# Kernel tuning notes

Hardware: AMD Instinct MI355X
Metric: run time of the kernel (lower is better)

The kernel has to match this reference:

```python
import jax, jax.numpy as jnp
import numpy as np

FEATURE_DIM, HIDDEN_DIM, ATTN_DIM = 2048, 1024, 1024
B, L = 128, 196


def setup_inputs() -> dict:
    key = jax.random.key(0)
    ks = jax.random.split(key, 8)
    s_enc = 1.0 / np.sqrt(FEATURE_DIM)
    s_hid = 1.0 / np.sqrt(HIDDEN_DIM)
    s_full = 1.0 / np.sqrt(ATTN_DIM)
    return {
        "encoder_out": jax.random.normal(ks[0], (B, L, FEATURE_DIM), jnp.float32),
        "hidden": jax.random.normal(ks[1], (B, HIDDEN_DIM), jnp.float32),
        "W_enc": jax.random.uniform(ks[2], (FEATURE_DIM, ATTN_DIM), jnp.float32, -s_enc, s_enc),
        "b_enc": jax.random.uniform(ks[3], (ATTN_DIM,), jnp.float32, -s_enc, s_enc),
        "W_hid": jax.random.uniform(ks[4], (HIDDEN_DIM, ATTN_DIM), jnp.float32, -s_hid, s_hid),
        "b_hid": jax.random.uniform(ks[5], (ATTN_DIM,), jnp.float32, -s_hid, s_hid),
        "W_full": jax.random.uniform(ks[6], (ATTN_DIM,), jnp.float32, -s_full, s_full),
        "b_full": jax.random.uniform(ks[7], (1,), jnp.float32, -s_full, s_full),
    }


def reference(encoder_out, hidden, W_enc, b_enc, W_hid, b_hid, W_full, b_full):
    # attn1: (B, L, A)
    attn1 = jnp.einsum("blf,fa->bla", encoder_out, W_enc) + b_enc
    # attn2: (B, 1, A)
    attn2 = (hidden @ W_hid + b_hid)[:, None, :]
    attn = jax.nn.relu(attn1 + attn2)
    # scalar score per location: (B, L)
    scores = jnp.einsum("bla,a->bl", attn, W_full) + b_full[0]
    alpha = jax.nn.softmax(scores, axis=1)
    # weighted sum over L: (B, F)
    context = jnp.einsum("blf,bl->bf", encoder_out, alpha)
    return context, alpha
```

## Files before the change

kernel.cpp:

```cpp
#include <hip/hip_runtime.h>
#include <hip/hip_bf16.h>

typedef unsigned short u16;
typedef short s16x8 __attribute__((ext_vector_type(8)));
typedef float f32x4 __attribute__((ext_vector_type(4)));

#define F_DIM 2048
#define A_DIM 1024
#define H_DIM 1024
#define BATCH 128
#define LLEN  196
#define MROWS (BATCH * LLEN)
#define LDA   40

__device__ __forceinline__ u16 f2b(float x) {
  union { float f; unsigned int u; } c; c.f = x;
  unsigned int r = (c.u + 0x7fffu + ((c.u >> 16) & 1u)) >> 16;
  return (u16)r;
}

__global__ void wenc_cvt_kernel(const float* __restrict__ W, u16* __restrict__ WT) {
  __shared__ float tile[32][33];
  int kb = blockIdx.x * 32, ab = blockIdx.y * 32;
  int t = threadIdx.x;
  int r = t >> 3, c = (t & 7) * 4;
  float4 v = *(const float4*)&W[(size_t)(kb + r) * A_DIM + ab + c];
  tile[r][c] = v.x; tile[r][c + 1] = v.y; tile[r][c + 2] = v.z; tile[r][c + 3] = v.w;
  __syncthreads();
  ushort4 o;
  o.x = f2b(tile[c + 0][r]);
  o.y = f2b(tile[c + 1][r]);
  o.z = f2b(tile[c + 2][r]);
  o.w = f2b(tile[c + 3][r]);
  *(ushort4*)&WT[(size_t)(ab + r) * F_DIM + kb + c] = o;
}

__global__ void attn2_kernel(const float* __restrict__ hidden, const float* __restrict__ W_hid,
                             const float* __restrict__ b_hid, const float* __restrict__ b_enc,
                             float* __restrict__ attn2p) {
  __shared__ float hl[8][256];
  int t = threadIdx.x;
  int a  = blockIdx.x * 256 + t;
  int b0 = blockIdx.y * 8;
  int k0 = blockIdx.z * 256;
  {
    int j = t >> 5, kk = (t & 31) * 8;
    float4 v0 = *(const float4*)&hidden[(size_t)(b0 + j) * H_DIM + k0 + kk];
    float4 v1 = *(const float4*)&hidden[(size_t)(b0 + j) * H_DIM + k0 + kk + 4];
    hl[j][kk + 0] = v0.x; hl[j][kk + 1] = v0.y; hl[j][kk + 2] = v0.z; hl[j][kk + 3] = v0.w;
    hl[j][kk + 4] = v1.x; hl[j][kk + 5] = v1.y; hl[j][kk + 6] = v1.z; hl[j][kk + 7] = v1.w;
  }
  __syncthreads();
  float acc[8] = {0.f, 0.f, 0.f, 0.f, 0.f, 0.f, 0.f, 0.f};
  #pragma unroll 4
  for (int k = 0; k < 256; ++k) {
    float w = W_hid[(size_t)(k0 + k) * A_DIM + a];
    #pragma unroll
    for (int j = 0; j < 8; ++j) acc[j] = fmaf(hl[j][k], w, acc[j]);
  }
  if (blockIdx.z == 0) {
    float bias = b_hid[a] + b_enc[a];
    #pragma unroll
    for (int j = 0; j < 8; ++j) acc[j] += bias;
  }
  #pragma unroll
  for (int j = 0; j < 8; ++j) atomicAdd(&attn2p[(size_t)(b0 + j) * A_DIM + a], acc[j]);
}

__global__ void gemm_score_kernel(const float* __restrict__ enc, const u16* __restrict__ WT,
                                  const float* __restrict__ attn2p, const float* __restrict__ W_full,
                                  float* __restrict__ scores) {
  __shared__ __align__(16) u16 As[128 * LDA];
  __shared__ __align__(16) u16 Bs[128 * LDA];
  __shared__ float wf_lds[128];
  __shared__ float at2_lds[2][128];

  int n0 = blockIdx.x * 128;
  int m0 = blockIdx.y * 128;
  int t = threadIdx.x;

  int b0 = m0 / LLEN;
  int bnd = (b0 + 1) * LLEN;
  int b1 = min(b0 + 1, BATCH - 1);

  if (t < 128) {
    wf_lds[t] = W_full[n0 + t];
    at2_lds[0][t] = attn2p[(size_t)b0 * A_DIM + n0 + t];
    at2_lds[1][t] = attn2p[(size_t)b1 * A_DIM + n0 + t];
  }

  int lane = t & 63, wave = t >> 6;
  int wr = wave >> 1, wc = wave & 1;
  int c16 = lane & 15, quad = lane >> 4;

  f32x4 acc[4][4];
  #pragma unroll
  for (int i = 0; i < 4; ++i)
    #pragma unroll
    for (int j = 0; j < 4; ++j) acc[i][j] = (f32x4){0.f, 0.f, 0.f, 0.f};

  int ar = t >> 3, ac = (t & 7) * 4;
  int br = t >> 2, bc = (t & 3) * 8;
  const float* ap = enc + (size_t)(m0 + ar) * F_DIM + ac;
  const u16*  bp = WT + (size_t)(n0 + br) * F_DIM + bc;

  for (int kt = 0; kt < F_DIM; kt += 32) {
    #pragma unroll
    for (int p = 0; p < 4; ++p) {
      float4 v = *(const float4*)(ap + (size_t)p * 32 * F_DIM + kt);
      ushort4 u;
      u.x = f2b(v.x); u.y = f2b(v.y); u.z = f2b(v.z); u.w = f2b(v.w);
      *(ushort4*)&As[(ar + p * 32) * LDA + ac] = u;
    }
    #pragma unroll
    for (int p = 0; p < 2; ++p) {
      uint4 v = *(const uint4*)(bp + (size_t)p * 64 * F_DIM + kt);
      *(uint4*)&Bs[(br + p * 64) * LDA + bc] = v;
    }
    __syncthreads();
    s16x8 af[4], bf[4];
    #pragma unroll
    for (int i = 0; i < 4; ++i) {
      af[i] = *(const s16x8*)&As[(wr * 64 + i * 16 + c16) * LDA + quad * 8];
      bf[i] = *(const s16x8*)&Bs[(wc * 64 + i * 16 + c16) * LDA + quad * 8];
    }
    #pragma unroll
    for (int mi = 0; mi < 4; ++mi)
      #pragma unroll
      for (int ni = 0; ni < 4; ++ni)
        acc[mi][ni] = __builtin_amdgcn_mfma_f32_16x16x32_bf16(af[mi], bf[ni], acc[mi][ni], 0, 0, 0);
    __syncthreads();
  }

  float wf[4], a2a[4], a2b[4];
  #pragma unroll
  for (int ni = 0; ni < 4; ++ni) {
    int col = wc * 64 + ni * 16 + c16;
    wf[ni] = wf_lds[col];
    a2a[ni] = at2_lds[0][col];
    a2b[ni] = at2_lds[1][col];
  }
  #pragma unroll
  for (int mi = 0; mi < 4; ++mi) {
    #pragma unroll
    for (int r = 0; r < 4; ++r) {
      int row_g = m0 + wr * 64 + mi * 16 + quad * 4 + r;
      bool hi = row_g >= bnd;
      float p = 0.f;
      #pragma unroll
      for (int ni = 0; ni < 4; ++ni) {
        float v = acc[mi][ni][r] + (hi ? a2b[ni] : a2a[ni]);
        v = fmaxf(v, 0.f);
        p = fmaf(v, wf[ni], p);
      }
      p += __shfl_xor(p, 1);
      p += __shfl_xor(p, 2);
      p += __shfl_xor(p, 4);
      p += __shfl_xor(p, 8);
      if (c16 == 0) atomicAdd(&scores[row_g], p);
    }
  }
}

__global__ void softmax_kernel(const float* __restrict__ scores, float* __restrict__ alpha) {
  __shared__ float red[8];
  int b = blockIdx.x, t = threadIdx.x;
  float s = (t < LLEN) ? scores[b * LLEN + t] : -3.0e38f;
  float m = s;
  #pragma unroll
  for (int o = 1; o <= 32; o <<= 1) m = fmaxf(m, __shfl_xor(m, o));
  if ((t & 63) == 0) red[t >> 6] = m;
  __syncthreads();
  m = fmaxf(fmaxf(red[0], red[1]), fmaxf(red[2], red[3]));
  float e = (t < LLEN) ? expf(s - m) : 0.f;
  float sum = e;
  #pragma unroll
  for (int o = 1; o <= 32; o <<= 1) sum += __shfl_xor(sum, o);
  __syncthreads();
  if ((t & 63) == 0) red[4 + (t >> 6)] = sum;
  __syncthreads();
  sum = red[4] + red[5] + red[6] + red[7];
  if (t < LLEN) alpha[b * LLEN + t] = e / sum;
}

__global__ void context_kernel(const float* __restrict__ enc, const float* __restrict__ alpha,
                               float* __restrict__ out) {
  __shared__ float al[LLEN];
  int b = blockIdx.y, t = threadIdx.x;
  int f4 = blockIdx.x * 256 + t;
  if (t < LLEN) al[t] = alpha[b * LLEN + t];
  __syncthreads();
  const float4* e4 = (const float4*)enc + (size_t)b * LLEN * (F_DIM / 4) + f4;
  float4 acc = {0.f, 0.f, 0.f, 0.f};
  #pragma unroll 4
  for (int l = 0; l < LLEN; ++l) {
    float4 v = e4[(size_t)l * (F_DIM / 4)];
    float a = al[l];
    acc.x = fmaf(v.x, a, acc.x);
    acc.y = fmaf(v.y, a, acc.y);
    acc.z = fmaf(v.z, a, acc.z);
    acc.w = fmaf(v.w, a, acc.w);
  }
  ((float4*)out)[(size_t)b * (F_DIM / 4) + f4] = acc;
}

extern "C" void kernel_launch(void* const* d_in, const int* in_sizes, int n_in,
                              void* d_out, int out_size, void* d_ws, size_t ws_size,
                              hipStream_t stream) {
  const float* enc    = (const float*)d_in[0];
  const float* hidden = (const float*)d_in[1];
  const float* W_enc  = (const float*)d_in[2];
  const float* b_enc  = (const float*)d_in[3];
  const float* W_hid  = (const float*)d_in[4];
  const float* b_hid  = (const float*)d_in[5];
  const float* W_full = (const float*)d_in[6];
  float* out = (float*)d_out;

  char* ws = (char*)d_ws;
  u16*   WT     = (u16*)ws;
  float* attn2p = (float*)(ws + (size_t)A_DIM * F_DIM * sizeof(u16));
  float* scores = (float*)(ws + (size_t)A_DIM * F_DIM * sizeof(u16) + (size_t)BATCH * A_DIM * sizeof(float));

  hipMemsetAsync(attn2p, 0, (size_t)BATCH * A_DIM * sizeof(float), stream);
  hipMemsetAsync(scores, 0, (size_t)MROWS * sizeof(float), stream);

  float* alpha_out = out + (size_t)BATCH * F_DIM;

  wenc_cvt_kernel<<<dim3(F_DIM / 32, A_DIM / 32), 256, 0, stream>>>(W_enc, WT);
  attn2_kernel<<<dim3(A_DIM / 256, BATCH / 8, 4), 256, 0, stream>>>(hidden, W_hid, b_hid, b_enc, attn2p);
  gemm_score_kernel<<<dim3(A_DIM / 128, MROWS / 128), 256, 0, stream>>>(enc, WT, attn2p, W_full, scores);
  softmax_kernel<<<dim3(BATCH), 256, 0, stream>>>(scores, alpha_out);
  context_kernel<<<dim3(F_DIM / 4 / 256, BATCH), 256, 0, stream>>>(enc, alpha_out, out);
}
```

Measured before the change: 575.3 us.

## Pre-convert encoder to bf16 and load GEMM tiles directly into LDS

Adds a pass that converts encoder_out to bf16 once into workspace, so the score GEMM no longer re-reads fp32 activations and converts them for every N-tile. The GEMM then uses global_load_lds to copy tiles straight into unpadded LDS. The context kernel is also split four ways over L and combined with atomics to expose more parallelism. This needs about 100MB of extra workspace, with a fallback to the old path if it is missing, and the unpadded LDS layout may cause bank conflicts.

```diff
diff --git a/kernel.cpp b/kernel.cpp
--- a/kernel.cpp
+++ b/kernel.cpp
@@ -19,6 +19,11 @@
   return (u16)r;
 }
 
+__device__ __forceinline__ void gload_lds16(const void* g, void* l) {
+  __builtin_amdgcn_global_load_lds((const __attribute__((address_space(1))) void*)g,
+                                   (__attribute__((address_space(3))) void*)l, 16, 0, 0);
+}
+
 __global__ void wenc_cvt_kernel(const float* __restrict__ W, u16* __restrict__ WT) {
   __shared__ float tile[32][33];
   int kb = blockIdx.x * 32, ab = blockIdx.y * 32;
@@ -33,6 +38,21 @@
   o.z = f2b(tile[c + 2][r]);
   o.w = f2b(tile[c + 3][r]);
   *(ushort4*)&WT[(size_t)(ab + r) * F_DIM + kb + c] = o;
+}
+
+__global__ void enc_cvt_kernel(const float* __restrict__ enc, u16* __restrict__ encb) {
+  int idx = blockIdx.x * 256 + threadIdx.x;
+  const float4* src = (const float4*)enc;
+  uint4* dst = (uint4*)encb;
+  #pragma unroll
+  for (int it = 0; it < 8; ++it) {
+    size_t p = (size_t)idx + (size_t)it * 802816;
+    float4 v0 = src[p * 2], v1 = src[p * 2 + 1];
+    union { u16 u[8]; uint4 q; } o;
+    o.u[0] = f2b(v0.x); o.u[1] = f2b(v0.y); o.u[2] = f2b(v0.z); o.u[3] = f2b(v0.w);
+    o.u[4] = f2b(v1.x); o.u[5] = f2b(v1.y); o.u[6] = f2b(v1.z); o.u[7] = f2b(v1.w);
+    dst[p] = o.q;
+  }
 }
 
 __global__ void attn2_kernel(const float* __restrict__ hidden, const float* __restrict__ W_hid,
@@ -67,11 +87,11 @@
   for (int j = 0; j < 8; ++j) atomicAdd(&attn2p[(size_t)(b0 + j) * A_DIM + a], acc[j]);
 }
 
-__global__ void gemm_score_kernel(const float* __restrict__ enc, const u16* __restrict__ WT,
-                                  const float* __restrict__ attn2p, const float* __restrict__ W_full,
-                                  float* __restrict__ scores) {
-  __shared__ __align__(16) u16 As[128 * LDA];
-  __shared__ __align__(16) u16 Bs[128 * LDA];
+__global__ void gemm_score_bf16(const u16* __restrict__ encb, const u16* __restrict__ WT,
+                                const float* __restrict__ attn2p, const float* __restrict__ W_full,
+                                float* __restrict__ scores) {
+  __shared__ __align__(16) u16 As[128 * 32];
+  __shared__ __align__(16) u16 Bs[128 * 32];
   __shared__ float wf_lds[128];
   __shared__ float at2_lds[2][128];
 
@@ -99,30 +119,24 @@
     #pragma unroll
     for (int j = 0; j < 4; ++j) acc[i][j] = (f32x4){0.f, 0.f, 0.f, 0.f};
 
-  int ar = t >> 3, ac = (t & 7) * 4;
-  int br = t >> 2, bc = (t & 3) * 8;
-  const float* ap = enc + (size_t)(m0 + ar) * F_DIM + ac;
-  const u16*  bp = WT + (size_t)(n0 + br) * F_DIM + bc;
+  const u16* agp0 = encb + (size_t)(m0 + (t >> 2)) * F_DIM + (t & 3) * 8;
+  const u16* agp1 = agp0 + (size_t)64 * F_DIM;
+  const u16* bgp0 = WT + (size_t)(n0 + (t >> 2)) * F_DIM + (t & 3) * 8;
+  const u16* bgp1 = bgp0 + (size_t)64 * F_DIM;
+  u16* al = As + wave * 512;
+  u16* bl = Bs + wave * 512;
 
   for (int kt = 0; kt < F_DIM; kt += 32) {
-    #pragma unroll
-    for (int p = 0; p < 4; ++p) {
-      float4 v = *(const float4*)(ap + (size_t)p * 32 * F_DIM + kt);
-      ushort4 u;
-      u.x = f2b(v.x); u.y = f2b(v.y); u.z = f2b(v.z); u.w = f2b(v.w);
-      *(ushort4*)&As[(ar + p * 32) * LDA + ac] = u;
-    }
-    #pragma unroll
-    for (int p = 0; p < 2; ++p) {
-      uint4 v = *(const uint4*)(bp + (size_t)p * 64 * F_DIM + kt);
-      *(uint4*)&Bs[(br + p * 64) * LDA + bc] = v;
-    }
+    gload_lds16(agp0 + kt, al);
+    gload_lds16(agp1 + kt, al + 2048);
+    gload_lds16(bgp0 + kt, bl);
+    gload_lds16(bgp1 + kt, bl + 2048);
     __syncthreads();
     s16x8 af[4], bf[4];
     #pragma unroll
     for (int i = 0; i < 4; ++i) {
-      af[i] = *(const s16x8*)&As[(wr * 64 + i * 16 + c16) * LDA + quad * 8];
-      bf[i] = *(const s16x8*)&Bs[(wc * 64 + i * 16 + c16) * LDA + quad * 8];
+      af[i] = *(const s16x8*)&As[(wr * 64 + i * 16 + c16) * 32 + quad * 8];
+      bf[i] = *(const s16x8*)&Bs[(wc * 64 + i * 16 + c16) * 32 + quad * 8];
     }
     #pragma unroll
     for (int mi = 0; mi < 4; ++mi)
@@ -162,6 +176,94 @@
   }
 }
 
+__global__ void gemm_score_f32(const float* __restrict__ enc, const u16* __restrict__ WT,
+                               const float* __restrict__ attn2p, const float* __restrict__ W_full,
+                               float* __restrict__ scores) {
+  __shared__ __align__(16) u16 As[128 * LDA];
+  __shared__ __align__(16) u16 Bs[128 * LDA];
+  __shared__ float wf_lds[128];
+  __shared__ float at2_lds[2][128];
+
+  int n0 = blockIdx.x * 128;
+  int m0 = blockIdx.y * 128;
+  int t = threadIdx.x;
+  int b0 = m0 / LLEN;
+  int bnd = (b0 + 1) * LLEN;
+  int b1 = min(b0 + 1, BATCH - 1);
+  if (t < 128) {
+    wf_lds[t] = W_full[n0 + t];
+    at2_lds[0][t] = attn2p[(size_t)b0 * A_DIM + n0 + t];
+    at2_lds[1][t] = attn2p[(size_t)b1 * A_DIM + n0 + t];
+  }
+  int lane = t & 63, wave = t >> 6;
+  int wr = wave >> 1, wc = wave & 1;
+  int c16 = lane & 15, quad = lane >> 4;
+  f32x4 acc[4][4];
+  #pragma unroll
+  for (int i = 0; i < 4; ++i)
+    #pragma unroll
+    for (int j = 0; j < 4; ++j) acc[i][j] = (f32x4){0.f, 0.f, 0.f, 0.f};
+  int ar = t >> 3, ac = (t & 7) * 4;
+  int br = t >> 2, bc = (t & 3) * 8;
+  const float* ap = enc + (size_t)(m0 + ar) * F_DIM + ac;
+  const u16*  bp = WT + (size_t)(n0 + br) * F_DIM + bc;
+  for (int kt = 0; kt < F_DIM; kt += 32) {
+    #pragma unroll
+    for (int p = 0; p < 4; ++p) {
+      float4 v = *(const float4*)(ap + (size_t)p * 32 * F_DIM + kt);
+      ushort4 u;
+      u.x = f2b(v.x); u.y = f2b(v.y); u.z = f2b(v.z); u.w = f2b(v.w);
+      *(ushort4*)&As[(ar + p * 32) * LDA + ac] = u;
+    }
+    #pragma unroll
+    for (int p = 0; p < 2; ++p) {
+      uint4 v = *(const uint4*)(bp + (size_t)p * 64 * F_DIM + kt);
+      *(uint4*)&Bs[(br + p * 64) * LDA + bc] = v;
+    }
+    __syncthreads();
+    s16x8 af[4], bf[4];
+    #pragma unroll
+    for (int i = 0; i < 4; ++i) {
+      af[i] = *(const s16x8*)&As[(wr * 64 + i * 16 + c16) * LDA + quad * 8];
+      bf[i] = *(const s16x8*)&Bs[(wc * 64 + i * 16 + c16) * LDA + quad * 8];
+    }
+    #pragma unroll
+    for (int mi = 0; mi < 4; ++mi)
+      #pragma unroll
+      for (int ni = 0; ni < 4; ++ni)
+        acc[mi][ni] = __builtin_amdgcn_mfma_f32_16x16x32_bf16(af[mi], bf[ni], acc[mi][ni], 0, 0, 0);
+    __syncthreads();
+  }
+  float wf[4], a2a[4], a2b[4];
+  #pragma unroll
+  for (int ni = 0; ni < 4; ++ni) {
+    int col = wc * 64 + ni * 16 + c16;
+    wf[ni] = wf_lds[col];
+    a2a[ni] = at2_lds[0][col];
+    a2b[ni] = at2_lds[1][col];
+  }
+  #pragma unroll
+  for (int mi = 0; mi < 4; ++mi) {
+    #pragma unroll
+    for (int r = 0; r < 4; ++r) {
+      int row_g = m0 + wr * 64 + mi * 16 + quad * 4 + r;
+      bool hi = row_g >= bnd;
+      float p = 0.f;
+      #pragma unroll
+      for (int ni = 0; ni < 4; ++ni) {
+        float v = acc[mi][ni][r] + (hi ? a2b[ni] : a2a[ni]);
+        v = fmaxf(v, 0.f);
+        p = fmaf(v, wf[ni], p);
+      }
+      p += __shfl_xor(p, 1);
+      p += __shfl_xor(p, 2);
+      p += __shfl_xor(p, 4);
+      p += __shfl_xor(p, 8);
+      if (c16 == 0) atomicAdd(&scores[row_g], p);
+    }
+  }
+}
+
 __global__ void softmax_kernel(const float* __restrict__ scores, float* __restrict__ alpha) {
   __shared__ float red[8];
   int b = blockIdx.x, t = threadIdx.x;
@@ -185,15 +287,16 @@
 
 __global__ void context_kernel(const float* __restrict__ enc, const float* __restrict__ alpha,
                                float* __restrict__ out) {
-  __shared__ float al[LLEN];
+  __shared__ float al[49];
   int b = blockIdx.y, t = threadIdx.x;
+  int l0 = blockIdx.z * 49;
   int f4 = blockIdx.x * 256 + t;
-  if (t < LLEN) al[t] = alpha[b * LLEN + t];
-  __syncthreads();
-  const float4* e4 = (const float4*)enc + (size_t)b * LLEN * (F_DIM / 4) + f4;
+  if (t < 49) al[t] = alpha[b * LLEN + l0 + t];
+  __syncthreads();
+  const float4* e4 = (const float4*)enc + ((size_t)b * LLEN + l0) * (F_DIM / 4) + f4;
   float4 acc = {0.f, 0.f, 0.f, 0.f};
-  #pragma unroll 4
-  for (int l = 0; l < LLEN; ++l) {
+  #pragma unroll 7
+  for (int l = 0; l < 49; ++l) {
     float4 v = e4[(size_t)l * (F_DIM / 4)];
     float a = al[l];
     acc.x = fmaf(v.x, a, acc.x);
@@ -201,7 +304,11 @@
     acc.z = fmaf(v.z, a, acc.z);
     acc.w = fmaf(v.w, a, acc.w);
   }
-  ((float4*)out)[(size_t)b * (F_DIM / 4) + f4] = acc;
+  float* o = out + (size_t)b * F_DIM + f4 * 4;
+  atomicAdd(o + 0, acc.x);
+  atomicAdd(o + 1, acc.y);
+  atomicAdd(o + 2, acc.z);
+  atomicAdd(o + 3, acc.w);
 }
 
 extern "C" void kernel_launch(void* const* d_in, const int* in_sizes, int n_in,
@@ -215,20 +322,43 @@
   const float* b_hid  = (const float*)d_in[5];
   const float* W_full = (const float*)d_in[6];
   float* out = (float*)d_out;
-
+  float* alpha_out = out + (size_t)BATCH * F_DIM;
+
+  const size_t encb_bytes = (size_t)MROWS * F_DIM * sizeof(u16);
+  const size_t wt_bytes   = (size_t)A_DIM * F_DIM * sizeof(u16);
+  const size_t a2_bytes   = (size_t)BATCH * A_DIM * sizeof(float);
+  const size_t sc_bytes   = (size_t)MROWS * sizeof(float);
   char* ws = (char*)d_ws;
-  u16*   WT     = (u16*)ws;
-  float* attn2p = (float*)(ws + (size_t)A_DIM * F_DIM * sizeof(u16));
-  float* scores = (float*)(ws + (size_t)A_DIM * F_DIM * sizeof(u16) + (size_t)BATCH * A_DIM * sizeof(float));
-
-  hipMemsetAsync(attn2p, 0, (size_t)BATCH * A_DIM * sizeof(float), stream);
-  hipMemsetAsync(scores, 0, (size_t)MROWS * sizeof(float), stream);
-
-  float* alpha_out = out + (size_t)BATCH * F_DIM;
-
-  wenc_cvt_kernel<<<dim3(F_DIM / 32, A_DIM / 32), 256, 0, stream>>>(W_enc, WT);
-  attn2_kernel<<<dim3(A_DIM / 256, BATCH / 8, 4), 256, 0, stream>>>(hidden, W_hid, b_hid, b_enc, attn2p);
-  gemm_score_kernel<<<dim3(A_DIM / 128, MROWS / 128), 256, 0, stream>>>(enc, WT, attn2p, W_full, scores);
-  softmax_kernel<<<dim3(BATCH), 256, 0, stream>>>(scores, alpha_out);
-  context_kernel<<<dim3(F_DIM / 4 / 256, BATCH), 256, 0, stream>>>(enc, alpha_out, out);
-}
+
+  if (ws_size >= encb_bytes + wt_bytes + a2_bytes + sc_bytes) {
+    u16*   encb   = (u16*)ws;
+    u16*   WT     = (u16*)(ws + encb_bytes);
+    float* attn2p = (float*)(ws + encb_bytes + wt_bytes);
+    float* scores = (float*)(ws + encb_bytes + wt_bytes + a2_bytes);
+
+    hipMemsetAsync(attn2p, 0, a2_bytes, stream);
+    hipMemsetAsync(scores, 0, sc_bytes, stream);
+    hipMemsetAsync(out, 0, (size_t)BATCH * F_DIM * sizeof(float), stream);
+
+    wenc_cvt_kernel<<<dim3(F_DIM / 32, A_DIM / 32), 256, 0, stream>>>(W_enc, WT);
+    enc_cvt_kernel<<<dim3(3136), 256, 0, stream>>>(enc, encb);
+    attn2_kernel<<<dim3(A_DIM / 256, BATCH / 8, 4), 256, 0, stream>>>(hidden, W_hid, b_hid, b_enc, attn2p);
+    gemm_score_bf16<<<dim3(A_DIM / 128, MROWS / 128), 256, 0, stream>>>(encb, WT, attn2p, W_full, scores);
+    softmax_kernel<<<dim3(BATCH), 256, 0, stream>>>(scores, alpha_out);
+    context_kernel<<<dim3(F_DIM / 4 / 256, BATCH, 4), 256, 0, stream>>>(enc, alpha_out, out);
+  } else {
+    u16*   WT     = (u16*)ws;
+    float* attn2p = (float*)(ws + wt_bytes);
+    float* scores = (float*)(ws + wt_bytes + a2_bytes);
+
+    hipMemsetAsync(attn2p, 0, a2_bytes, stream);
+    hipMemsetAsync(scores, 0, sc_bytes, stream);
+    hipMemsetAsync(out, 0, (size_t)BATCH * F_DIM * sizeof(float), stream);
+
+    wenc_cvt_kernel<<<dim3(F_DIM / 32, A_DIM / 32), 256, 0, stream>>>(W_enc, WT);
+    attn2_kernel<<<dim3(A_DIM / 256, BATCH / 8, 4), 256, 0, stream>>>(hidden, W_hid, b_hid, b_enc, attn2p);
+    gemm_score_f32<<<dim3(A_DIM / 128, MROWS / 128), 256, 0, stream>>>(enc, WT, attn2p, W_full, scores);
+    softmax_kernel<<<dim3(BATCH), 256, 0, stream>>>(scores, alpha_out);
+    context_kernel<<<dim3(F_DIM / 4 / 256, BATCH, 4), 256, 0, stream>>>(enc, alpha_out, out);
+  }
+}
```

After: 534.4 us. -7.1%, faster.
